# Kernel tuning notes

Measured on AMD Instinct MI355X. Metric: run time of the kernel, lower is better.

Reference implementation:

```python
import jax, jax.numpy as jnp
import numpy as np

T, B, OBS = 64, 2048, 512
H1, H2 = 400, 300
CORE = H2 + 1 + 1  # fc2 out + clipped_reward + last_action = 302


def setup_inputs() -> dict:
    key = jax.random.key(0)
    ks = jax.random.split(key, 12)
    s = lambda fan_in: 1.0 / np.sqrt(fan_in)
    return {
        "frame": jax.random.normal(ks[0], (T, B, OBS), jnp.float32),
        "reward": jax.random.normal(ks[1], (T, B), jnp.float32),
        "last_action": jax.random.randint(ks[2], (T, B), 0, 2, jnp.int64 if jax.config.jax_enable_x64 else jnp.int32),
        "eps": jax.random.normal(ks[3], (T * B,), jnp.float32),
        "W1": jax.random.uniform(ks[4], (H1, OBS), jnp.float32, -s(OBS), s(OBS)),
        "b1": jax.random.uniform(ks[5], (H1,), jnp.float32, -s(OBS), s(OBS)),
        "W2": jax.random.uniform(ks[6], (H2, H1), jnp.float32, -s(H1), s(H1)),
        "b2": jax.random.uniform(ks[7], (H2,), jnp.float32, -s(H1), s(H1)),
        "Wp": jax.random.uniform(ks[8], (2, CORE), jnp.float32, -s(CORE), s(CORE)),
        "bp": jax.random.uniform(ks[9], (2,), jnp.float32, -s(CORE), s(CORE)),
        "Wb": jax.random.uniform(ks[10], (1, CORE), jnp.float32, -s(CORE), s(CORE)),
        "bb": jax.random.uniform(ks[11], (1,), jnp.float32, -s(CORE), s(CORE)),
    }


def reference(frame, reward, last_action, eps, W1, b1, W2, b2, Wp, bp, Wb, bb):
    TB = T * B
    x = frame.reshape(TB, OBS)
    x = jax.nn.relu(x @ W1.T + b1)          # [TB, 400]
    x = jax.nn.relu(x @ W2.T + b2)          # [TB, 300]
    la = last_action.reshape(TB, 1).astype(jnp.float32)
    cr = jnp.clip(reward, -1.0, 1.0).reshape(TB, 1)
    core = jnp.concatenate([x, cr, la], axis=-1)  # [TB, 302]
    pl = jax.nn.sigmoid(core @ Wp.T + bp)   # [TB, 2] -> (mu, sigma)
    baseline = core @ Wb.T + bb             # [TB, 1]
    # vectorized Normal(mu, sigma).sample(); torch .sample() is detached
    action = jax.lax.stop_gradient(pl[:, 0] + pl[:, 1] * eps)  # [TB]
    out = jnp.concatenate(
        [pl.reshape(T, B, 2), baseline.reshape(T, B, 1), action.reshape(T, B, 1)],
        axis=-1,
    )  # [T, B, 4] = (policy_logits[2], baseline, action)
    return out
```

## Files before the change

### kernel.cpp

```cpp
#include <hip/hip_runtime.h>
#include <math.h>

#define TBR  131072
#define OBS  512
#define H1N  400
#define H2N  300
#define CORE 302

#define CH_K   64
#define NCHUNK 8
#define CH_S   72
#define H1_S   424
#define CO_S   328
#define WH_R   64

typedef __bf16 bf16x8 __attribute__((ext_vector_type(8)));
typedef float  f32x4  __attribute__((ext_vector_type(4)));

__device__ __forceinline__ bf16x8 cvt8(float4 a, float4 b) {
    bf16x8 v;
    v[0] = (__bf16)a.x; v[1] = (__bf16)a.y; v[2] = (__bf16)a.z; v[3] = (__bf16)a.w;
    v[4] = (__bf16)b.x; v[5] = (__bf16)b.y; v[6] = (__bf16)b.z; v[7] = (__bf16)b.w;
    return v;
}

__global__ void conv_weights(const float* __restrict__ W1,
                             const float* __restrict__ W2,
                             __bf16* __restrict__ ws) {
    const int n1 = (H1N * OBS) / 8;
    const int n2 = (H2N * H1N) / 8;
    int i = blockIdx.x * blockDim.x + threadIdx.x;
    if (i < n1) {
        const float4* p = reinterpret_cast<const float4*>(W1 + (size_t)i * 8);
        *reinterpret_cast<bf16x8*>(ws + (size_t)i * 8) = cvt8(p[0], p[1]);
    } else if (i < n1 + n2) {
        int j = i - n1;
        const float4* p = reinterpret_cast<const float4*>(W2 + (size_t)j * 8);
        *reinterpret_cast<bf16x8*>(ws + (size_t)(H1N * OBS) + (size_t)j * 8) =
            cvt8(p[0], p[1]);
    }
}

template <bool WBF16>
__global__ __launch_bounds__(512, 4) void autoprune_mfma(
    const float* __restrict__ frame, const float* __restrict__ reward,
    const int*   __restrict__ last_action, const float* __restrict__ eps,
    const float* __restrict__ W1f, const float* __restrict__ b1,
    const float* __restrict__ W2f, const float* __restrict__ b2,
    const float* __restrict__ Wp, const float* __restrict__ bp,
    const float* __restrict__ Wb, const float* __restrict__ bb,
    const __bf16* __restrict__ W1b, const __bf16* __restrict__ W2b,
    float* __restrict__ out)
{
    __shared__ __bf16 sm_chunk[2][64 * CH_S];
    __shared__ __bf16 sm_h1[64 * H1_S];
    __shared__ float  sm_res[64][4];
    __bf16* sm_core = sm_h1;

    const int tid  = threadIdx.x;
    const int w    = tid >> 6;
    const int l    = tid & 63;
    const int l15  = l & 15;
    const int lg   = l >> 4;
    const int row0 = blockIdx.x * 64;

    const int sr = tid >> 3;
    const int sc = (tid & 7) * 8;
    const float* fbase = frame + (size_t)(row0 + sr) * OBS + sc;

    {
        float4 a = *reinterpret_cast<const float4*>(fbase);
        float4 b = *reinterpret_cast<const float4*>(fbase + 4);
        if (tid < 192) {
            int r = tid / 3, c = 400 + (tid % 3) * 8;
            bf16x8 z;
            #pragma unroll
            for (int j = 0; j < 8; ++j) z[j] = (__bf16)0.0f;
            *reinterpret_cast<bf16x8*>(&sm_h1[r * H1_S + c]) = z;
        }
        *reinterpret_cast<bf16x8*>(&sm_chunk[0][sr * CH_S + sc]) = cvt8(a, b);
    }
    __syncthreads();

    {
        f32x4 acc[4][4];
        #pragma unroll
        for (int a = 0; a < 4; ++a)
            #pragma unroll
            for (int b = 0; b < 4; ++b) acc[a][b] = (f32x4){0.f, 0.f, 0.f, 0.f};

        for (int c = 0; c < NCHUNK; ++c) {
            float4 pa, pb;
            if (c < NCHUNK - 1) {
                pa = *reinterpret_cast<const float4*>(fbase + (c + 1) * CH_K);
                pb = *reinterpret_cast<const float4*>(fbase + (c + 1) * CH_K + 4);
            }
            const __bf16* buf = sm_chunk[c & 1];
            #pragma unroll
            for (int ks = 0; ks < 2; ++ks) {
                const int kl = ks * 32 + lg * 8;
                bf16x8 afr[4];
                #pragma unroll
                for (int mt = 0; mt < 4; ++mt)
                    afr[mt] = *reinterpret_cast<const bf16x8*>(
                        &buf[(mt * 16 + l15) * CH_S + kl]);
                const int kg = c * CH_K + kl;
                #pragma unroll
                for (int ti = 0; ti < 4; ++ti) {
                    int nt = w + ti * 8;
                    if (nt < 25) {
                        bf16x8 bfr;
                        if constexpr (WBF16) {
                            bfr = *reinterpret_cast<const bf16x8*>(
                                W1b + (size_t)(nt * 16 + l15) * OBS + kg);
                        } else {
                            const float4* wp = reinterpret_cast<const float4*>(
                                W1f + (size_t)(nt * 16 + l15) * OBS + kg);
                            bfr = cvt8(wp[0], wp[1]);
                        }
                        #pragma unroll
                        for (int mt = 0; mt < 4; ++mt)
                            acc[ti][mt] = __builtin_amdgcn_mfma_f32_16x16x32_bf16(
                                afr[mt], bfr, acc[ti][mt], 0, 0, 0);
                    }
                }
            }
            if (c < NCHUNK - 1)
                *reinterpret_cast<bf16x8*>(
                    &sm_chunk[(c + 1) & 1][sr * CH_S + sc]) = cvt8(pa, pb);
            __syncthreads();
        }

        #pragma unroll
        for (int ti = 0; ti < 4; ++ti) {
            int nt = w + ti * 8;
            if (nt < 25) {
                int c = nt * 16 + l15;
                float bias = b1[c];
                #pragma unroll
                for (int mt = 0; mt < 4; ++mt)
                    #pragma unroll
                    for (int j = 0; j < 4; ++j) {
                        int r = mt * 16 + lg * 4 + j;
                        sm_h1[r * H1_S + c] =
                            (__bf16)fmaxf(acc[ti][mt][j] + bias, 0.0f);
                    }
            }
        }
    }
    __syncthreads();

    f32x4 acc2[3][4];
    #pragma unroll
    for (int a = 0; a < 3; ++a)
        #pragma unroll
        for (int b = 0; b < 4; ++b) acc2[a][b] = (f32x4){0.f, 0.f, 0.f, 0.f};

    for (int ks = 0; ks < 13; ++ks) {
        const int kb = ks * 32 + lg * 8;
        bf16x8 afr[4];
        #pragma unroll
        for (int mt = 0; mt < 4; ++mt)
            afr[mt] = *reinterpret_cast<const bf16x8*>(
                &sm_h1[(mt * 16 + l15) * H1_S + kb]);
        const int kbw = (kb >= 400) ? 0 : kb;
        #pragma unroll
        for (int ti = 0; ti < 3; ++ti) {
            int nt = w + ti * 8;
            if (nt < 19) {
                int cc = nt * 16 + l15;
                if (cc >= 300) cc = 299;
                bf16x8 bfr;
                if constexpr (WBF16) {
                    bfr = *reinterpret_cast<const bf16x8*>(
                        W2b + (size_t)cc * H1N + kbw);
                } else {
                    const float4* wp = reinterpret_cast<const float4*>(
                        W2f + (size_t)cc * H1N + kbw);
                    bfr = cvt8(wp[0], wp[1]);
                }
                #pragma unroll
                for (int mt = 0; mt < 4; ++mt)
                    acc2[ti][mt] = __builtin_amdgcn_mfma_f32_16x16x32_bf16(
                        afr[mt], bfr, acc2[ti][mt], 0, 0, 0);
            }
        }
    }
    __syncthreads();

    #pragma unroll
    for (int ti = 0; ti < 3; ++ti) {
        int nt = w + ti * 8;
        if (nt < 19) {
            int c = nt * 16 + l15;
            if (c < 300) {
                float bias = b2[c];
                #pragma unroll
                for (int mt = 0; mt < 4; ++mt)
                    #pragma unroll
                    for (int j = 0; j < 4; ++j) {
                        int r = mt * 16 + lg * 4 + j;
                        sm_core[r * CO_S + c] =
                            (__bf16)fmaxf(acc2[ti][mt][j] + bias, 0.0f);
                    }
            }
        }
    }
    if (tid < 64) {
        int r = row0 + tid;
        float cr = fminf(fmaxf(reward[r], -1.0f), 1.0f);
        sm_core[tid * CO_S + 300] = (__bf16)cr;
        sm_core[tid * CO_S + 301] = (__bf16)(float)last_action[r];
        #pragma unroll
        for (int k = 302; k < 320; ++k) sm_core[tid * CO_S + k] = (__bf16)0.0f;
    }
    for (int i = tid; i < 3 * CO_S; i += 512) {
        int ro = i / CO_S, k = i - ro * CO_S;
        float v = (k < CORE) ? ((ro < 2) ? Wp[ro * CORE + k] : Wb[k]) : 0.0f;
        sm_core[(WH_R + ro) * CO_S + k] = (__bf16)v;
    }
    __syncthreads();

    if (w < 4) {
        f32x4 hac = (f32x4){0.f, 0.f, 0.f, 0.f};
        #pragma unroll
        for (int ks = 0; ks < 10; ++ks) {
            int kb = ks * 32 + lg * 8;
            bf16x8 afr = *reinterpret_cast<const bf16x8*>(
                &sm_core[(w * 16 + l15) * CO_S + kb]);
            bf16x8 bfr = *reinterpret_cast<const bf16x8*>(
                &sm_core[(WH_R + l15) * CO_S + kb]);
            hac = __builtin_amdgcn_mfma_f32_16x16x32_bf16(afr, bfr, hac, 0, 0, 0);
        }
        if (l15 < 3) {
            float bias = (l15 < 2) ? bp[l15] : bb[0];
            #pragma unroll
            for (int j = 0; j < 4; ++j) {
                float v = hac[j] + bias;
                if (l15 < 2) v = 1.0f / (1.0f + __expf(-v));
                sm_res[w * 16 + lg * 4 + j][l15] = v;
            }
        }
    }
    __syncthreads();

    if (tid < 64) {
        int r = row0 + tid;
        float mu = sm_res[tid][0], sg = sm_res[tid][1], bl = sm_res[tid][2];
        float4 o4 = make_float4(mu, sg, bl, fmaf(sg, eps[r], mu));
        *reinterpret_cast<float4*>(out + (size_t)r * 4) = o4;
    }
}

extern "C" void kernel_launch(void* const* d_in, const int* in_sizes, int n_in,
                              void* d_out, int out_size, void* d_ws, size_t ws_size,
                              hipStream_t stream) {
    const float* frame       = (const float*)d_in[0];
    const float* reward      = (const float*)d_in[1];
    const int*   last_action = (const int*)  d_in[2];
    const float* eps         = (const float*)d_in[3];
    const float* W1          = (const float*)d_in[4];
    const float* b1          = (const float*)d_in[5];
    const float* W2          = (const float*)d_in[6];
    const float* b2          = (const float*)d_in[7];
    const float* Wp          = (const float*)d_in[8];
    const float* bp          = (const float*)d_in[9];
    const float* Wb          = (const float*)d_in[10];
    const float* bb          = (const float*)d_in[11];
    float* out = (float*)d_out;

    const size_t wbytes = (size_t)(H1N * OBS + H2N * H1N) * 2;
    dim3 grid(TBR / 64);

    if (ws_size >= wbytes) {
        __bf16* wsb = (__bf16*)d_ws;
        int nconv = (H1N * OBS + H2N * H1N) / 8;
        conv_weights<<<(nconv + 255) / 256, 256, 0, stream>>>(W1, W2, wsb);
        autoprune_mfma<true><<<grid, 512, 0, stream>>>(
            frame, reward, last_action, eps, W1, b1, W2, b2, Wp, bp, Wb, bb,
            (const __bf16*)wsb, (const __bf16*)(wsb + H1N * OBS), out);
    } else {
        autoprune_mfma<false><<<grid, 512, 0, stream>>>(
            frame, reward, last_action, eps, W1, b1, W2, b2, Wp, bp, Wb, bb,
            (const __bf16*)nullptr, (const __bf16*)nullptr, out);
    }
}
```

Measured before the change: 184.2 us.

## Load frame A-fragments directly from global, drop LDS staging and extra syncs

Removes the double-buffered LDS staging of frame chunks in the first GEMM. Each lane now loads its A-fragment from global memory and converts it to bf16 in registers, which also removes the per-chunk __syncthreads. The head weights are read straight from global instead of being staged in shared memory, the final reduction writes outputs via shuffles instead of a shared result buffer, and the loops are partially unrolled. This lowers LDS footprint and barrier count, which may raise occupancy. The cost is that frame rows are read with a less coalesced pattern: each lane reads 32 bytes from a different row, and every warp re-reads the same A data.

```diff
diff --git a/kernel.cpp b/kernel.cpp
--- a/kernel.cpp
+++ b/kernel.cpp
@@ -7,14 +7,10 @@
 #define H2N  300
 #define CORE 302
 
-#define CH_K   64
-#define NCHUNK 8
-#define CH_S   72
-#define H1_S   424
-#define CO_S   328
-#define WH_R   64
+#define H1_S 424
 
 typedef __bf16 bf16x8 __attribute__((ext_vector_type(8)));
+typedef __bf16 bf16x4 __attribute__((ext_vector_type(4)));
 typedef float  f32x4  __attribute__((ext_vector_type(4)));
 
 __device__ __forceinline__ bf16x8 cvt8(float4 a, float4 b) {
@@ -52,35 +48,21 @@
     const __bf16* __restrict__ W1b, const __bf16* __restrict__ W2b,
     float* __restrict__ out)
 {
-    __shared__ __bf16 sm_chunk[2][64 * CH_S];
     __shared__ __bf16 sm_h1[64 * H1_S];
-    __shared__ float  sm_res[64][4];
-    __bf16* sm_core = sm_h1;
 
     const int tid  = threadIdx.x;
     const int w    = tid >> 6;
-    const int l    = tid & 63;
-    const int l15  = l & 15;
-    const int lg   = l >> 4;
+    const int l15  = tid & 15;
+    const int lg   = (tid & 63) >> 4;
     const int row0 = blockIdx.x * 64;
 
-    const int sr = tid >> 3;
-    const int sc = (tid & 7) * 8;
-    const float* fbase = frame + (size_t)(row0 + sr) * OBS + sc;
-
-    {
-        float4 a = *reinterpret_cast<const float4*>(fbase);
-        float4 b = *reinterpret_cast<const float4*>(fbase + 4);
-        if (tid < 192) {
-            int r = tid / 3, c = 400 + (tid % 3) * 8;
-            bf16x8 z;
-            #pragma unroll
-            for (int j = 0; j < 8; ++j) z[j] = (__bf16)0.0f;
-            *reinterpret_cast<bf16x8*>(&sm_h1[r * H1_S + c]) = z;
-        }
-        *reinterpret_cast<bf16x8*>(&sm_chunk[0][sr * CH_S + sc]) = cvt8(a, b);
-    }
-    __syncthreads();
+    if (tid < 192) {
+        int r = tid / 3, c = 400 + (tid % 3) * 8;
+        bf16x8 z;
+        #pragma unroll
+        for (int j = 0; j < 8; ++j) z[j] = (__bf16)0.0f;
+        *reinterpret_cast<bf16x8*>(&sm_h1[r * H1_S + c]) = z;
+    }
 
     {
         f32x4 acc[4][4];
@@ -89,46 +71,38 @@
             #pragma unroll
             for (int b = 0; b < 4; ++b) acc[a][b] = (f32x4){0.f, 0.f, 0.f, 0.f};
 
-        for (int c = 0; c < NCHUNK; ++c) {
-            float4 pa, pb;
-            if (c < NCHUNK - 1) {
-                pa = *reinterpret_cast<const float4*>(fbase + (c + 1) * CH_K);
-                pb = *reinterpret_cast<const float4*>(fbase + (c + 1) * CH_K + 4);
-            }
-            const __bf16* buf = sm_chunk[c & 1];
-            #pragma unroll
-            for (int ks = 0; ks < 2; ++ks) {
-                const int kl = ks * 32 + lg * 8;
-                bf16x8 afr[4];
-                #pragma unroll
-                for (int mt = 0; mt < 4; ++mt)
-                    afr[mt] = *reinterpret_cast<const bf16x8*>(
-                        &buf[(mt * 16 + l15) * CH_S + kl]);
-                const int kg = c * CH_K + kl;
-                #pragma unroll
-                for (int ti = 0; ti < 4; ++ti) {
-                    int nt = w + ti * 8;
-                    if (nt < 25) {
-                        bf16x8 bfr;
-                        if constexpr (WBF16) {
-                            bfr = *reinterpret_cast<const bf16x8*>(
-                                W1b + (size_t)(nt * 16 + l15) * OBS + kg);
-                        } else {
-                            const float4* wp = reinterpret_cast<const float4*>(
-                                W1f + (size_t)(nt * 16 + l15) * OBS + kg);
-                            bfr = cvt8(wp[0], wp[1]);
-                        }
-                        #pragma unroll
-                        for (int mt = 0; mt < 4; ++mt)
-                            acc[ti][mt] = __builtin_amdgcn_mfma_f32_16x16x32_bf16(
-                                afr[mt], bfr, acc[ti][mt], 0, 0, 0);
+        const float* arow0 = frame + (size_t)(row0 + l15) * OBS;
+
+        #pragma unroll 2
+        for (int ks = 0; ks < 16; ++ks) {
+            const int kb = ks * 32 + lg * 8;
+            bf16x8 afr[4];
+            #pragma unroll
+            for (int mt = 0; mt < 4; ++mt) {
+                const float* ap = arow0 + (size_t)(mt * 16) * OBS + kb;
+                float4 f0 = *reinterpret_cast<const float4*>(ap);
+                float4 f1 = *reinterpret_cast<const float4*>(ap + 4);
+                afr[mt] = cvt8(f0, f1);
+            }
+            #pragma unroll
+            for (int ti = 0; ti < 4; ++ti) {
+                int nt = w + ti * 8;
+                if (nt < 25) {
+                    bf16x8 bfr;
+                    if constexpr (WBF16) {
+                        bfr = *reinterpret_cast<const bf16x8*>(
+                            W1b + (size_t)(nt * 16 + l15) * OBS + kb);
+                    } else {
+                        const float4* wp = reinterpret_cast<const float4*>(
+                            W1f + (size_t)(nt * 16 + l15) * OBS + kb);
+                        bfr = cvt8(wp[0], wp[1]);
                     }
+                    #pragma unroll
+                    for (int mt = 0; mt < 4; ++mt)
+                        acc[ti][mt] = __builtin_amdgcn_mfma_f32_16x16x32_bf16(
+                            afr[mt], bfr, acc[ti][mt], 0, 0, 0);
                 }
             }
-            if (c < NCHUNK - 1)
-                *reinterpret_cast<bf16x8*>(
-                    &sm_chunk[(c + 1) & 1][sr * CH_S + sc]) = cvt8(pa, pb);
-            __syncthreads();
         }
 
         #pragma unroll
@@ -156,6 +130,7 @@
         #pragma unroll
         for (int b = 0; b < 4; ++b) acc2[a][b] = (f32x4){0.f, 0.f, 0.f, 0.f};
 
+    #pragma unroll 2
     for (int ks = 0; ks < 13; ++ks) {
         const int kb = ks * 32 + lg * 8;
         bf16x8 afr[4];
@@ -200,7 +175,7 @@
                     #pragma unroll
                     for (int j = 0; j < 4; ++j) {
                         int r = mt * 16 + lg * 4 + j;
-                        sm_core[r * CO_S + c] =
+                        sm_h1[r * H1_S + c] =
                             (__bf16)fmaxf(acc2[ti][mt][j] + bias, 0.0f);
                     }
             }
@@ -209,46 +184,52 @@
     if (tid < 64) {
         int r = row0 + tid;
         float cr = fminf(fmaxf(reward[r], -1.0f), 1.0f);
-        sm_core[tid * CO_S + 300] = (__bf16)cr;
-        sm_core[tid * CO_S + 301] = (__bf16)(float)last_action[r];
-        #pragma unroll
-        for (int k = 302; k < 320; ++k) sm_core[tid * CO_S + k] = (__bf16)0.0f;
-    }
-    for (int i = tid; i < 3 * CO_S; i += 512) {
-        int ro = i / CO_S, k = i - ro * CO_S;
-        float v = (k < CORE) ? ((ro < 2) ? Wp[ro * CORE + k] : Wb[k]) : 0.0f;
-        sm_core[(WH_R + ro) * CO_S + k] = (__bf16)v;
+        bf16x4 tail;
+        tail[0] = (__bf16)cr;
+        tail[1] = (__bf16)(float)last_action[r];
+        tail[2] = (__bf16)0.0f;
+        tail[3] = (__bf16)0.0f;
+        *reinterpret_cast<bf16x4*>(&sm_h1[tid * H1_S + 300]) = tail;
+        bf16x8 z;
+        #pragma unroll
+        for (int j = 0; j < 8; ++j) z[j] = (__bf16)0.0f;
+        *reinterpret_cast<bf16x8*>(&sm_h1[tid * H1_S + 304]) = z;
+        *reinterpret_cast<bf16x8*>(&sm_h1[tid * H1_S + 312]) = z;
     }
     __syncthreads();
 
     if (w < 4) {
         f32x4 hac = (f32x4){0.f, 0.f, 0.f, 0.f};
+        const float* wsrc = (l15 == 2) ? Wb : (Wp + l15 * CORE);
         #pragma unroll
         for (int ks = 0; ks < 10; ++ks) {
             int kb = ks * 32 + lg * 8;
             bf16x8 afr = *reinterpret_cast<const bf16x8*>(
-                &sm_core[(w * 16 + l15) * CO_S + kb]);
-            bf16x8 bfr = *reinterpret_cast<const bf16x8*>(
-                &sm_core[(WH_R + l15) * CO_S + kb]);
+                &sm_h1[(w * 16 + l15) * H1_S + kb]);
+            bf16x8 bfr;
+            #pragma unroll
+            for (int e = 0; e < 8; ++e) {
+                int k = kb + e;
+                bfr[e] = (l15 < 3 && k < CORE) ? (__bf16)wsrc[k] : (__bf16)0.0f;
+            }
             hac = __builtin_amdgcn_mfma_f32_16x16x32_bf16(afr, bfr, hac, 0, 0, 0);
         }
-        if (l15 < 3) {
-            float bias = (l15 < 2) ? bp[l15] : bb[0];
-            #pragma unroll
-            for (int j = 0; j < 4; ++j) {
-                float v = hac[j] + bias;
-                if (l15 < 2) v = 1.0f / (1.0f + __expf(-v));
-                sm_res[w * 16 + lg * 4 + j][l15] = v;
-            }
-        }
-    }
-    __syncthreads();
-
-    if (tid < 64) {
-        int r = row0 + tid;
-        float mu = sm_res[tid][0], sg = sm_res[tid][1], bl = sm_res[tid][2];
-        float4 o4 = make_float4(mu, sg, bl, fmaf(sg, eps[r], mu));
-        *reinterpret_cast<float4*>(out + (size_t)r * 4) = o4;
+        float bias = (l15 == 0) ? bp[0] : (l15 == 1) ? bp[1] : (l15 == 2) ? bb[0] : 0.0f;
+        #pragma unroll
+        for (int j = 0; j < 4; ++j) {
+            float v = hac[j] + bias;
+            if (l15 < 2) v = 1.0f / (1.0f + __expf(-v));
+            float ot = __shfl_xor(v, 1);
+            int r = row0 + w * 16 + lg * 4 + j;
+            if (l15 == 0) {
+                out[(size_t)r * 4 + 0] = v;
+                out[(size_t)r * 4 + 3] = fmaf(ot, eps[r], v);
+            } else if (l15 == 1) {
+                out[(size_t)r * 4 + 1] = v;
+            } else if (l15 == 2) {
+                out[(size_t)r * 4 + 2] = v;
+            }
+        }
     }
 }
 
```

Result: slower. 420.1 us (+128.0%).
